# Optimization experiments

Hardware: AMD Instinct MI355X
Metric: run time of the kernel (lower is better)

## Reference

```python
import jax, jax.numpy as jnp
import numpy as np

B, N = 32, 1024  # batch, square grid size (Ny == Nx forced by expand_as in the torch module)


def setup_inputs() -> dict:
    key = jax.random.key(0)
    k1, k2, k3 = jax.random.split(key, 3)
    xaxis = jnp.arange(N, dtype=jnp.float32)            # sorted knot positions along x
    yaxis = jnp.arange(N, dtype=jnp.float32)            # sorted knot positions along y
    signal = jax.random.normal(k1, (B, N, N), dtype=jnp.float32)
    # queries constrained to [0.5, N-3] so gathered indices I+1 stay in-bounds for the
    # (N-1)-length slope tensors, matching the valid-domain assumption of the torch code
    xs = jax.random.uniform(k2, (N,), minval=0.5, maxval=float(N - 3), dtype=jnp.float32)
    ys = jax.random.uniform(k3, (N,), minval=0.5, maxval=float(N - 3), dtype=jnp.float32)
    return {"xaxis": xaxis, "yaxis": yaxis, "signal": signal, "xs": xs, "ys": ys}


def _h_poly(t):
    # Cubic Hermite basis: rows of A = [[1,0,-3,2],[0,1,-2,1],[0,0,3,-2],[0,0,-1,1]] dotted with [1,t,t^2,t^3]
    t2 = t * t
    t3 = t2 * t
    h0 = 1.0 - 3.0 * t2 + 2.0 * t3
    h1 = t - 2.0 * t2 + t3
    h2 = 3.0 * t2 - 2.0 * t3
    h3 = t3 - t2
    return h0, h1, h2, h3


def _interp1d(inp, axis1d, m, q):
    # inp: [..., N] values, m: [..., N-1] slopes, axis1d: [N] shared knots, q: [M] queries
    # torch.searchsorted(x0[...,1:-1], xs) with right=False == jnp.searchsorted side='left'
    I = jnp.searchsorted(axis1d[1:-1], q)          # [M], int
    x = axis1d[I]                                  # [M]
    dx = axis1d[I + 1] - x                         # [M]
    t = (q - x) / dx                               # [M]
    h0, h1, h2, h3 = _h_poly(t)

    def g(a, idx):
        idx_b = jnp.broadcast_to(idx, a.shape[:-1] + idx.shape)
        return jnp.take_along_axis(a, idx_b, axis=-1)

    return (h0 * g(inp, I)
            + h1 * g(m, I) * dx
            + h2 * g(inp, I + 1)
            + h3 * g(m, I + 1) * dx)


def reference(xaxis, yaxis, signal, xs, ys):
    # slopes (x1/x2 are just the 1D axes broadcast over signal, so diffs reduce to 1D diffs)
    m1 = (signal[..., 1:] - signal[..., :-1]) / (xaxis[1:] - xaxis[:-1])        # [B,N,N-1]
    sT = jnp.swapaxes(signal, -2, -1)
    m2 = (sT[..., 1:] - sT[..., :-1]) / (yaxis[1:] - yaxis[:-1])                # [B,N,N-1]
    out = jnp.swapaxes(_interp1d(signal, xaxis, m1, xs), -2, -1)                # [B,Mx,N]
    out = jnp.swapaxes(_interp1d(out, yaxis, m2, ys), -2, -1)                   # [B,My,N]
    return out
```

## Files before the change

### kernel.cpp

```cpp
#include <hip/hip_runtime.h>


#define NGRID 1024
#define BATCH 32
#define KB    4

typedef float nfloat4 __attribute__((ext_vector_type(4)));

__global__ __launch_bounds__(256) void hermite2d_fused(
    const float* __restrict__ signal,
    const float* __restrict__ xs,
    const float* __restrict__ ys,
    float* __restrict__ out)
{
    const unsigned f = blockIdx.x;
    const int xcd = (int)(f & 7u);
    const int k   = (int)(f >> 3);
    const int b0  = xcd * KB;
    const int t   = threadIdx.x;

    __shared__ float crow[KB][NGRID];

    const float qy = ys[k];
    int Iy = (int)floorf(qy);
    if (Iy < 0) Iy = 0;
    if (Iy > NGRID - 3) Iy = NGRID - 3;
    const float ty  = qy - (float)Iy;
    const float ty2 = ty * ty;
    const float ty3 = ty2 * ty;
    const float h0y = 1.0f - 3.0f * ty2 + 2.0f * ty3;
    const float h1y = ty - 2.0f * ty2 + ty3;
    const float h2y = 3.0f * ty2 - 2.0f * ty3;
    const float h3y = ty3 - ty2;

    float colp[KB][4];
    #pragma unroll
    for (int i = 0; i < KB; ++i) {
        const float4* src4 =
            (const float4*)(signal + ((size_t)(b0 + i) * NGRID + (size_t)Iy) * NGRID);
        const float4 r0 = src4[t];
        const float4 r1 = src4[t + NGRID / 4];
        const float4 r2 = src4[t + NGRID / 2];

        float4 c;
        c.x = h0y * r0.x + h2y * r1.x;
        c.y = h0y * r0.y + h2y * r1.y;
        c.z = h0y * r0.z + h2y * r1.z;
        c.w = h0y * r0.w + h2y * r1.w;
        ((float4*)crow[i])[t] = c;

        colp[i][0] = h1y * (r1.x - r0.x) + h3y * (r2.x - r1.x);
        colp[i][1] = h1y * (r1.y - r0.y) + h3y * (r2.y - r1.y);
        colp[i][2] = h1y * (r1.z - r0.z) + h3y * (r2.z - r1.z);
        colp[i][3] = h1y * (r1.w - r0.w) + h3y * (r2.w - r1.w);
    }

    const float4 q4 = ((const float4*)xs)[t];
    const float qx[4] = { q4.x, q4.y, q4.z, q4.w };

    __syncthreads();

    float4 res[KB];
    #pragma unroll
    for (int j = 0; j < 4; ++j) {
        const float q = qx[j];
        int Ix = (int)floorf(q);
        if (Ix < 0) Ix = 0;
        if (Ix > NGRID - 3) Ix = NGRID - 3;
        const float tx = q - (float)Ix;
        const float t2 = tx * tx;
        const float t3 = t2 * tx;
        const float w0 = 1.0f - tx - t2 + t3;
        const float w1 = tx + 2.0f * (t2 - t3);
        const float w2 = t3 - t2;
        #pragma unroll
        for (int i = 0; i < KB; ++i) {
            const float c0 = crow[i][Ix];
            const float c1 = crow[i][Ix + 1];
            const float c2 = crow[i][Ix + 2];
            ((float*)&res[i])[j] = w0 * c0 + w1 * c1 + w2 * c2 + colp[i][j];
        }
    }

    #pragma unroll
    for (int i = 0; i < KB; ++i) {
        nfloat4* orow4 = (nfloat4*)(out + ((size_t)(b0 + i) * NGRID + (size_t)k) * NGRID);
        __builtin_nontemporal_store(*(const nfloat4*)&res[i], &orow4[t]);
    }
}

extern "C" void kernel_launch(void* const* d_in, const int* in_sizes, int n_in,
                              void* d_out, int out_size, void* d_ws, size_t ws_size,
                              hipStream_t stream) {
    const float* signal = (const float*)d_in[2];
    const float* xs     = (const float*)d_in[3];
    const float* ys     = (const float*)d_in[4];
    float* out          = (float*)d_out;

    dim3 grid(NGRID * (BATCH / KB));
    hermite2d_fused<<<grid, 256, 0, stream>>>(signal, xs, ys, out);
}
```

Before: 255.4 us.

## Assign one batch per wavefront and drop block-wide barrier

Restructures the work split so each 64-lane wavefront owns one batch image and loops over four column chunks, instead of each thread covering all four batches for one column chunk. Because every wavefront reads only the shared row it wrote, the block-level barrier is removed, relying on intra-wavefront LDS ordering. An occupancy hint is added to launch bounds. Intended to cut synchronization stalls and register pressure, at the cost of relying on wave-synchronous visibility of shared-memory writes.

```diff
diff --git a/kernel.cpp b/kernel.cpp
--- a/kernel.cpp
+++ b/kernel.cpp
@@ -7,17 +7,18 @@
 
 typedef float nfloat4 __attribute__((ext_vector_type(4)));
 
-__global__ __launch_bounds__(256) void hermite2d_fused(
+__global__ __launch_bounds__(256, 6) void hermite2d_fused(
     const float* __restrict__ signal,
     const float* __restrict__ xs,
     const float* __restrict__ ys,
     float* __restrict__ out)
 {
     const unsigned f = blockIdx.x;
-    const int xcd = (int)(f & 7u);
-    const int k   = (int)(f >> 3);
-    const int b0  = xcd * KB;
-    const int t   = threadIdx.x;
+    const int xcd  = (int)(f & 7u);
+    const int k    = (int)(f >> 3);
+    const int w    = threadIdx.x >> 6;
+    const int lane = threadIdx.x & 63;
+    const int b    = xcd * KB + w;
 
     __shared__ float crow[KB][NGRID];
 
@@ -33,59 +34,55 @@
     const float h2y = 3.0f * ty2 - 2.0f * ty3;
     const float h3y = ty3 - ty2;
 
+    const float4* src4 =
+        (const float4*)(signal + ((size_t)b * NGRID + (size_t)Iy) * NGRID);
+
     float colp[KB][4];
     #pragma unroll
-    for (int i = 0; i < KB; ++i) {
-        const float4* src4 =
-            (const float4*)(signal + ((size_t)(b0 + i) * NGRID + (size_t)Iy) * NGRID);
-        const float4 r0 = src4[t];
-        const float4 r1 = src4[t + NGRID / 4];
-        const float4 r2 = src4[t + NGRID / 2];
+    for (int c = 0; c < 4; ++c) {
+        const int s = c * 64 + lane;
+        const float4 r0 = src4[s];
+        const float4 r1 = src4[s + NGRID / 4];
+        const float4 r2 = src4[s + NGRID / 2];
 
-        float4 c;
-        c.x = h0y * r0.x + h2y * r1.x;
-        c.y = h0y * r0.y + h2y * r1.y;
-        c.z = h0y * r0.z + h2y * r1.z;
-        c.w = h0y * r0.w + h2y * r1.w;
-        ((float4*)crow[i])[t] = c;
+        float4 cc;
+        cc.x = h0y * r0.x + h2y * r1.x;
+        cc.y = h0y * r0.y + h2y * r1.y;
+        cc.z = h0y * r0.z + h2y * r1.z;
+        cc.w = h0y * r0.w + h2y * r1.w;
+        ((float4*)crow[w])[s] = cc;
 
-        colp[i][0] = h1y * (r1.x - r0.x) + h3y * (r2.x - r1.x);
-        colp[i][1] = h1y * (r1.y - r0.y) + h3y * (r2.y - r1.y);
-        colp[i][2] = h1y * (r1.z - r0.z) + h3y * (r2.z - r1.z);
-        colp[i][3] = h1y * (r1.w - r0.w) + h3y * (r2.w - r1.w);
+        colp[c][0] = h1y * (r1.x - r0.x) + h3y * (r2.x - r1.x);
+        colp[c][1] = h1y * (r1.y - r0.y) + h3y * (r2.y - r1.y);
+        colp[c][2] = h1y * (r1.z - r0.z) + h3y * (r2.z - r1.z);
+        colp[c][3] = h1y * (r1.w - r0.w) + h3y * (r2.w - r1.w);
     }
 
-    const float4 q4 = ((const float4*)xs)[t];
-    const float qx[4] = { q4.x, q4.y, q4.z, q4.w };
 
-    __syncthreads();
-
-    float4 res[KB];
+    float* orow = out + ((size_t)b * NGRID + (size_t)k) * NGRID;
     #pragma unroll
-    for (int j = 0; j < 4; ++j) {
-        const float q = qx[j];
-        int Ix = (int)floorf(q);
-        if (Ix < 0) Ix = 0;
-        if (Ix > NGRID - 3) Ix = NGRID - 3;
-        const float tx = q - (float)Ix;
-        const float t2 = tx * tx;
-        const float t3 = t2 * tx;
-        const float w0 = 1.0f - tx - t2 + t3;
-        const float w1 = tx + 2.0f * (t2 - t3);
-        const float w2 = t3 - t2;
+    for (int c = 0; c < 4; ++c) {
+        const int s = c * 64 + lane;
+        const float4 q4 = ((const float4*)xs)[s];
+        float4 res;
         #pragma unroll
-        for (int i = 0; i < KB; ++i) {
-            const float c0 = crow[i][Ix];
-            const float c1 = crow[i][Ix + 1];
-            const float c2 = crow[i][Ix + 2];
-            ((float*)&res[i])[j] = w0 * c0 + w1 * c1 + w2 * c2 + colp[i][j];
+        for (int j = 0; j < 4; ++j) {
+            const float q = ((const float*)&q4)[j];
+            int Ix = (int)floorf(q);
+            if (Ix < 0) Ix = 0;
+            if (Ix > NGRID - 3) Ix = NGRID - 3;
+            const float tx = q - (float)Ix;
+            const float t2 = tx * tx;
+            const float t3 = t2 * tx;
+            const float w0 = 1.0f - tx - t2 + t3;
+            const float w1 = tx + 2.0f * (t2 - t3);
+            const float w2 = t3 - t2;
+            const float c0 = crow[w][Ix];
+            const float c1 = crow[w][Ix + 1];
+            const float c2 = crow[w][Ix + 2];
+            ((float*)&res)[j] = w0 * c0 + w1 * c1 + w2 * c2 + colp[c][j];
         }
-    }
-
-    #pragma unroll
-    for (int i = 0; i < KB; ++i) {
-        nfloat4* orow4 = (nfloat4*)(out + ((size_t)(b0 + i) * NGRID + (size_t)k) * NGRID);
-        __builtin_nontemporal_store(*(const nfloat4*)&res[i], &orow4[t]);
+        __builtin_nontemporal_store(*(const nfloat4*)&res, (nfloat4*)orow + s);
     }
 }
 
```

After: 258.5 us. About the same (+1.2%).
